# Kernel tuning notes

Measured on AMD Instinct MI355X. Metric: run time of the kernel, lower is better.

The kernel has to match this reference:

```python
import jax, jax.numpy as jnp
import numpy as np

N_NODES = 50000
IN_DIM = 256
LATENT = 128
HIDDEN = 2 * LATENT  # 256


def _xavier(key, fan_in, fan_out):
    # matches nn.init.xavier_uniform_ on a [out, in] weight; we store as [in, out]
    limit = float(np.sqrt(6.0 / (fan_in + fan_out)))
    return jax.random.uniform(key, (fan_in, fan_out), jnp.float32, -limit, limit)


def setup_inputs() -> dict:
    key = jax.random.key(0)
    ks = jax.random.split(key, 8)
    x = jax.random.normal(ks[0], (N_NODES, IN_DIM), jnp.float32)
    edge_index = jax.random.randint(ks[1], (2, 800000), 0, N_NODES, jnp.int64)
    W1 = _xavier(ks[2], IN_DIM, HIDDEN)
    b1 = jnp.zeros((HIDDEN,), jnp.float32)
    Wmu = _xavier(ks[3], HIDDEN, LATENT)
    bmu = jnp.zeros((LATENT,), jnp.float32)
    Wlv = _xavier(ks[4], HIDDEN, LATENT)
    blv = jnp.zeros((LATENT,), jnp.float32)
    return {"x": x, "edge_index": edge_index, "W1": W1, "b1": b1,
            "Wmu": Wmu, "bmu": bmu, "Wlv": Wlv, "blv": blv}


def _gcn_layer(x, W, b, src, dst):
    # PyG GCNConv: h = x @ W; add self loops; symmetric norm; scatter-add; + bias
    h = x @ W  # [N, out]
    ones = jnp.ones(src.shape[0], x.dtype)
    deg = jax.ops.segment_sum(ones, dst, num_segments=N_NODES) + 1.0  # +1 for self loop
    dinv = jax.lax.rsqrt(deg)  # deg >= 1 always
    norm = dinv[src] * dinv[dst]  # [E]
    agg = jax.ops.segment_sum(h[src] * norm[:, None], dst, num_segments=N_NODES)
    agg = agg + h * (dinv * dinv)[:, None]  # self-loop contribution, norm_ii = 1/deg_i
    return agg + b


def reference(x, edge_index, W1, b1, Wmu, bmu, Wlv, blv):
    src, dst = edge_index[0], edge_index[1]
    z = _gcn_layer(x, W1, b1, src, dst)
    z = jax.nn.relu(z)
    # dropout in eval mode == identity
    mu = _gcn_layer(z, Wmu, bmu, src, dst)
    logvar = _gcn_layer(z, Wlv, blv, src, dst)
    return (mu, logvar)
```

## Files before the change

### kernel.cpp

```cpp
#include <hip/hip_runtime.h>

#define N_NODES 50000
#define E_EDGES 800000
#define D 256
#define L 128
#define CAP 64

typedef __attribute__((ext_vector_type(8))) short bf16x8;
typedef __attribute__((ext_vector_type(4))) float f32x4;

__device__ __forceinline__ float bf2f(unsigned short u) {
    union { unsigned int i; float f; } v; v.i = ((unsigned int)u) << 16; return v.f;
}
__device__ __forceinline__ unsigned short f2bf(float f) {
    union { float f; unsigned int i; } v; v.f = f;
    unsigned int r = v.i + 0x7fffu + ((v.i >> 16) & 1u);
    return (unsigned short)(r >> 16);
}

__global__ __launch_bounds__(256) void zero_i(int* __restrict__ p, int n) {
    int i = blockIdx.x * 256 + threadIdx.x;
    if (i < n) p[i] = 0;
}

__global__ __launch_bounds__(256) void fill_fixed(const int* __restrict__ src,
                                                  const int* __restrict__ dst,
                                                  int* __restrict__ cursor,
                                                  int* __restrict__ bucket) {
    int e = blockIdx.x * 256 + threadIdx.x;
    if (e >= E_EDGES) return;
    int d = dst[e];
    int pos = atomicAdd(&cursor[d], 1);
    if (pos < CAP) bucket[d * CAP + pos] = src[e];
}

__global__ __launch_bounds__(256) void dinv_fin(const int* __restrict__ cursor,
                                                float* __restrict__ dinv) {
    int i = blockIdx.x * 256 + threadIdx.x;
    if (i < N_NODES) dinv[i] = rsqrtf((float)cursor[i] + 1.0f);
}

__global__ __launch_bounds__(256) void prep_w(
    const float* __restrict__ W1, const float* __restrict__ Wmu,
    const float* __restrict__ Wlv, const float* __restrict__ bmu,
    const float* __restrict__ blv,
    unsigned short* __restrict__ W1h, unsigned short* __restrict__ W1l,
    unsigned short* __restrict__ Wch, unsigned short* __restrict__ Wcl,
    float* __restrict__ bcat) {
    int b = blockIdx.x, t = threadIdx.x;
    if (b < 256) {
        int n = b, k = t;
        float w = W1[k * 256 + n];
        unsigned short h = f2bf(w);
        W1h[n * 256 + k] = h;
        W1l[n * 256 + k] = f2bf(w - bf2f(h));
    } else {
        int n = b - 256, k = t;
        float w = (n < 128) ? Wmu[k * 128 + n] : Wlv[k * 128 + (n - 128)];
        unsigned short h = f2bf(w);
        Wch[n * 256 + k] = h;
        Wcl[n * 256 + k] = f2bf(w - bf2f(h));
        if (b == 256) bcat[t] = (t < 128) ? bmu[t] : blv[t - 128];
    }
}

__global__ __launch_bounds__(256, 3) void gemm_mfma(
    const float* __restrict__ A,
    const unsigned short* __restrict__ Bth, const unsigned short* __restrict__ Btl,
    unsigned short* __restrict__ Hout,
    float* __restrict__ mu, float* __restrict__ lv,
    const float* __restrict__ bias, int M, int mode)
{
    __shared__ unsigned short Bsh[256 * 32];
    __shared__ unsigned short Bsl[256 * 32];
    const int t = threadIdx.x;
    const int lane = t & 63, wave = t >> 6;
    const int row0 = blockIdx.x * 64 + wave * 16;
    const int m_ = lane & 15, q = lane >> 4;
    int rA = row0 + m_; if (rA >= M) rA = M - 1;
    const float* Ap = A + (size_t)rA * 256;
    const int bn = t >> 2;
    const int bc = t & 3;

    f32x4 acc[16];
    const f32x4 zf = {0.f, 0.f, 0.f, 0.f};
#pragma unroll
    for (int nt = 0; nt < 16; ++nt) acc[nt] = zf;

    for (int ks = 0; ks < 8; ++ks) {
        const int k0 = ks * 32;
        bf16x8 gbh[4], gbl[4];
#pragma unroll
        for (int i = 0; i < 4; ++i) {
            int n = bn + i * 64;
            gbh[i] = *(const bf16x8*)(Bth + n * 256 + k0 + bc * 8);
            gbl[i] = *(const bf16x8*)(Btl + n * 256 + k0 + bc * 8);
        }
        float4 av0 = *(const float4*)(Ap + k0 + q * 8);
        float4 av1 = *(const float4*)(Ap + k0 + q * 8 + 4);
        __syncthreads();
#pragma unroll
        for (int i = 0; i < 4; ++i) {
            int n = bn + i * 64;
            int cc = (bc ^ ((n >> 1) & 3)) * 8;
            *(bf16x8*)&Bsh[n * 32 + cc] = gbh[i];
            *(bf16x8*)&Bsl[n * 32 + cc] = gbl[i];
        }
        float af[8] = {av0.x, av0.y, av0.z, av0.w, av1.x, av1.y, av1.z, av1.w};
        bf16x8 ah, al;
#pragma unroll
        for (int j = 0; j < 8; ++j) {
            unsigned short h = f2bf(af[j]);
            ah[j] = (short)h;
            al[j] = (short)f2bf(af[j] - bf2f(h));
        }
        __syncthreads();
#pragma unroll
        for (int nt = 0; nt < 16; ++nt) {
            int n = nt * 16 + m_;
            int cr = (q ^ ((n >> 1) & 3)) * 8;
            bf16x8 bh = *(const bf16x8*)&Bsh[n * 32 + cr];
            bf16x8 bl = *(const bf16x8*)&Bsl[n * 32 + cr];
            acc[nt] = __builtin_amdgcn_mfma_f32_16x16x32_bf16(ah, bh, acc[nt], 0, 0, 0);
            acc[nt] = __builtin_amdgcn_mfma_f32_16x16x32_bf16(ah, bl, acc[nt], 0, 0, 0);
            acc[nt] = __builtin_amdgcn_mfma_f32_16x16x32_bf16(al, bh, acc[nt], 0, 0, 0);
        }
    }
    int rbase = row0 + q * 4;
#pragma unroll
    for (int r = 0; r < 4; ++r) {
        int grow = rbase + r;
        if (grow >= M) continue;
#pragma unroll
        for (int nt = 0; nt < 16; ++nt) {
            int gcol = nt * 16 + m_;
            float v = acc[nt][r];
            if (mode == 0) {
                Hout[(size_t)grow * 256 + gcol] = f2bf(v);
            } else {
                v += bias[gcol];
                if (gcol < 128) mu[(size_t)grow * 128 + gcol] = v;
                else            lv[(size_t)grow * 128 + (gcol - 128)] = v;
            }
        }
    }
}

__global__ __launch_bounds__(256) void gather_pre(
    const unsigned short* __restrict__ Hs,
    const int* __restrict__ bucket, const int* __restrict__ cnt_,
    const float* __restrict__ dinv, const float* __restrict__ bias,
    unsigned short* __restrict__ OutZ, float* __restrict__ OutY, int mode)
{
    const int lane = threadIdx.x & 63;
    const int hl = lane & 31;
    const int bb = lane & 32;
    const int node = blockIdx.x * 8 + (threadIdx.x >> 5);
    const int col = hl * 8;
    int cnt = cnt_[node]; if (cnt > CAP) cnt = CAP;
    float dn = dinv[node];

    int   s0r = 0, s1r = 0;
    float w0r = 0.f, w1r = 0.f;
    if (hl < cnt)      { s0r = bucket[node * CAP + hl];      w0r = dinv[s0r] * dn; }
    if (hl + 32 < cnt) { s1r = bucket[node * CAP + 32 + hl]; w1r = dinv[s1r] * dn; }

    float sl = dn * dn;
    bf16x8 hv = *(const bf16x8*)(Hs + (size_t)node * D + col);
    float a[8];
#pragma unroll
    for (int p = 0; p < 8; ++p) a[p] = bf2f((unsigned short)hv[p]) * sl;

    const int cnt0 = cnt < 32 ? cnt : 32;
    int j = 0;
    for (; j + 3 < cnt0; j += 4) {
        int t0 = __shfl(s0r, bb + j,     64), t1 = __shfl(s0r, bb + j + 1, 64);
        int t2 = __shfl(s0r, bb + j + 2, 64), t3 = __shfl(s0r, bb + j + 3, 64);
        float w0 = __shfl(w0r, bb + j,     64), w1 = __shfl(w0r, bb + j + 1, 64);
        float w2 = __shfl(w0r, bb + j + 2, 64), w3 = __shfl(w0r, bb + j + 3, 64);
        bf16x8 u0 = *(const bf16x8*)(Hs + (size_t)t0 * D + col);
        bf16x8 u1 = *(const bf16x8*)(Hs + (size_t)t1 * D + col);
        bf16x8 u2 = *(const bf16x8*)(Hs + (size_t)t2 * D + col);
        bf16x8 u3 = *(const bf16x8*)(Hs + (size_t)t3 * D + col);
#pragma unroll
        for (int p = 0; p < 8; ++p) a[p] = fmaf(bf2f((unsigned short)u0[p]), w0, a[p]);
#pragma unroll
        for (int p = 0; p < 8; ++p) a[p] = fmaf(bf2f((unsigned short)u1[p]), w1, a[p]);
#pragma unroll
        for (int p = 0; p < 8; ++p) a[p] = fmaf(bf2f((unsigned short)u2[p]), w2, a[p]);
#pragma unroll
        for (int p = 0; p < 8; ++p) a[p] = fmaf(bf2f((unsigned short)u3[p]), w3, a[p]);
    }
    for (; j < cnt0; ++j) {
        int   t0 = __shfl(s0r, bb + j, 64);
        float w0 = __shfl(w0r, bb + j, 64);
        bf16x8 u0 = *(const bf16x8*)(Hs + (size_t)t0 * D + col);
#pragma unroll
        for (int p = 0; p < 8; ++p) a[p] = fmaf(bf2f((unsigned short)u0[p]), w0, a[p]);
    }
    if (cnt > 32) {
        for (int j2 = 0; j2 < cnt - 32; ++j2) {
            int   t0 = __shfl(s1r, bb + j2, 64);
            float w0 = __shfl(w1r, bb + j2, 64);
            bf16x8 u0 = *(const bf16x8*)(Hs + (size_t)t0 * D + col);
#pragma unroll
            for (int p = 0; p < 8; ++p) a[p] = fmaf(bf2f((unsigned short)u0[p]), w0, a[p]);
        }
    }

    if (mode == 0) {
        float4 b0 = *(const float4*)(bias + col);
        float4 b1 = *(const float4*)(bias + col + 4);
        float bf[8] = {b0.x, b0.y, b0.z, b0.w, b1.x, b1.y, b1.z, b1.w};
        bf16x8 o;
#pragma unroll
        for (int p = 0; p < 8; ++p) o[p] = (short)f2bf(fmaxf(a[p] + bf[p], 0.f));
        *(bf16x8*)(OutZ + (size_t)node * D + col) = o;
    } else {
        float4 o0, o1;
        o0.x = a[0]; o0.y = a[1]; o0.z = a[2]; o0.w = a[3];
        o1.x = a[4]; o1.y = a[5]; o1.z = a[6]; o1.w = a[7];
        float* Yp = OutY + (size_t)node * D + col;
        *(float4*)Yp = o0;
        *(float4*)(Yp + 4) = o1;
    }
}

extern "C" void kernel_launch(void* const* d_in, const int* in_sizes, int n_in,
                              void* d_out, int out_size, void* d_ws, size_t ws_size,
                              hipStream_t stream) {
    const float* x   = (const float*)d_in[0];
    const int*   ei  = (const int*)d_in[1];
    const float* W1  = (const float*)d_in[2];
    const float* b1  = (const float*)d_in[3];
    const float* Wmu = (const float*)d_in[4];
    const float* bmu = (const float*)d_in[5];
    const float* Wlv = (const float*)d_in[6];
    const float* blv = (const float*)d_in[7];
    const int* src = ei;
    const int* dst = ei + E_EDGES;

    const size_t NF = (size_t)N_NODES * D;
    unsigned short* Hb = (unsigned short*)d_ws;
    unsigned short* Z  = Hb + NF;
    float* Y = (float*)(Z + NF);
    unsigned short* W1h = (unsigned short*)(Y + NF);
    unsigned short* W1l = W1h + 65536;
    unsigned short* Wch = W1l + 65536;
    unsigned short* Wcl = Wch + 65536;
    float* bcat = (float*)(Wcl + 65536);
    float* dinv = bcat + 256;
    int* cursor = (int*)(dinv + N_NODES);
    int* bucket = cursor + N_NODES;
    float* mu = (float*)d_out;
    float* lv = mu + (size_t)N_NODES * L;

    zero_i<<<(N_NODES + 255) / 256, 256, 0, stream>>>(cursor, N_NODES);
    fill_fixed<<<(E_EDGES + 255) / 256, 256, 0, stream>>>(src, dst, cursor, bucket);
    dinv_fin<<<(N_NODES + 255) / 256, 256, 0, stream>>>(cursor, dinv);

    prep_w<<<512, 256, 0, stream>>>(W1, Wmu, Wlv, bmu, blv, W1h, W1l, Wch, Wcl, bcat);

    const int gemm_blocks = (N_NODES + 63) / 64;
    const int gat_blocks  = N_NODES / 8;
    gemm_mfma<<<gemm_blocks, 256, 0, stream>>>(x, W1h, W1l, Hb,
                                               nullptr, nullptr, nullptr, N_NODES, 0);
    gather_pre<<<gat_blocks, 256, 0, stream>>>(Hb, bucket, cursor, dinv, b1,
                                               Z, nullptr, 0);
    gather_pre<<<gat_blocks, 256, 0, stream>>>(Z, bucket, cursor, dinv, nullptr,
                                               nullptr, Y, 1);
    gemm_mfma<<<gemm_blocks, 256, 0, stream>>>(Y, Wch, Wcl, nullptr,
                                               mu, lv, bcat, N_NODES, 1);
}
```

Baseline: 345.3 us.

## Column-slice gather with packed fp16 edge weights in bucket entries

```diff
diff --git a/kernel.cpp b/kernel.cpp
--- a/kernel.cpp
+++ b/kernel.cpp
@@ -5,6 +5,7 @@
 #define D 256
 #define L 128
 #define CAP 64
+#define SCOL 32
 
 typedef __attribute__((ext_vector_type(8))) short bf16x8;
 typedef __attribute__((ext_vector_type(4))) float f32x4;
@@ -16,6 +17,17 @@
     union { float f; unsigned int i; } v; v.f = f;
     unsigned int r = v.i + 0x7fffu + ((v.i >> 16) & 1u);
     return (unsigned short)(r >> 16);
+}
+__device__ __forceinline__ unsigned short f2h(float f) {
+    union { float f; unsigned int i; } v; v.f = f;
+    unsigned int r = v.i - 0x38000000u;
+    r = r + 0xfffu + ((r >> 13) & 1u);
+    return (unsigned short)(r >> 13);
+}
+__device__ __forceinline__ float h2f(unsigned int u) {
+    union { unsigned int i; float f; } v;
+    v.i = ((u & 0x7fffu) << 13) + 0x38000000u;
+    return v.f;
 }
 
 __global__ __launch_bounds__(256) void zero_i(int* __restrict__ p, int n) {
@@ -38,6 +50,21 @@
                                                 float* __restrict__ dinv) {
     int i = blockIdx.x * 256 + threadIdx.x;
     if (i < N_NODES) dinv[i] = rsqrtf((float)cursor[i] + 1.0f);
+}
+
+__global__ __launch_bounds__(256) void pack_bucket(int* __restrict__ bucket,
+                                                   const int* __restrict__ cnt_,
+                                                   const float* __restrict__ dinv) {
+    int node = blockIdx.x * 4 + (threadIdx.x >> 6);
+    if (node >= N_NODES) return;
+    int lane = threadIdx.x & 63;
+    int cnt = cnt_[node]; if (cnt > CAP) cnt = CAP;
+    if (lane < cnt) {
+        int idx = node * CAP + lane;
+        int s = bucket[idx];
+        unsigned short wh = f2h(dinv[s] * dinv[node]);
+        bucket[idx] = (s & 0xffff) | ((int)wh << 16);
+    }
 }
 
 __global__ __launch_bounds__(256) void prep_w(
@@ -146,42 +173,41 @@
     }
 }
 
-__global__ __launch_bounds__(256) void gather_pre(
+__global__ __launch_bounds__(256) void gather_slice(
     const unsigned short* __restrict__ Hs,
-    const int* __restrict__ bucket, const int* __restrict__ cnt_,
+    const int* __restrict__ epk, const int* __restrict__ cnt_,
     const float* __restrict__ dinv, const float* __restrict__ bias,
     unsigned short* __restrict__ OutZ, float* __restrict__ OutY, int mode)
 {
-    const int lane = threadIdx.x & 63;
-    const int hl = lane & 31;
-    const int bb = lane & 32;
-    const int node = blockIdx.x * 8 + (threadIdx.x >> 5);
-    const int col = hl * 8;
+    const int s = blockIdx.x & 7;
+    const int g = blockIdx.x >> 3;
+    const int t = threadIdx.x;
+    const int node = g * 64 + ((t >> 6) << 4) + ((t & 63) >> 2);
+    if (node >= N_NODES) return;
+    const int r = t & 3;
+    const int col = s * SCOL + r * 8;
     int cnt = cnt_[node]; if (cnt > CAP) cnt = CAP;
-    float dn = dinv[node];
-
-    int   s0r = 0, s1r = 0;
-    float w0r = 0.f, w1r = 0.f;
-    if (hl < cnt)      { s0r = bucket[node * CAP + hl];      w0r = dinv[s0r] * dn; }
-    if (hl + 32 < cnt) { s1r = bucket[node * CAP + 32 + hl]; w1r = dinv[s1r] * dn; }
-
-    float sl = dn * dn;
-    bf16x8 hv = *(const bf16x8*)(Hs + (size_t)node * D + col);
+    const float dn = dinv[node];
+    const unsigned short* Hp = Hs + col;
+
     float a[8];
-#pragma unroll
-    for (int p = 0; p < 8; ++p) a[p] = bf2f((unsigned short)hv[p]) * sl;
-
-    const int cnt0 = cnt < 32 ? cnt : 32;
+    {
+        bf16x8 hv = *(const bf16x8*)(Hp + (size_t)node * D);
+        float sl = dn * dn;
+#pragma unroll
+        for (int p = 0; p < 8; ++p) a[p] = bf2f((unsigned short)hv[p]) * sl;
+    }
+
+    const int* ep = epk + node * CAP;
     int j = 0;
-    for (; j + 3 < cnt0; j += 4) {
-        int t0 = __shfl(s0r, bb + j,     64), t1 = __shfl(s0r, bb + j + 1, 64);
-        int t2 = __shfl(s0r, bb + j + 2, 64), t3 = __shfl(s0r, bb + j + 3, 64);
-        float w0 = __shfl(w0r, bb + j,     64), w1 = __shfl(w0r, bb + j + 1, 64);
-        float w2 = __shfl(w0r, bb + j + 2, 64), w3 = __shfl(w0r, bb + j + 3, 64);
-        bf16x8 u0 = *(const bf16x8*)(Hs + (size_t)t0 * D + col);
-        bf16x8 u1 = *(const bf16x8*)(Hs + (size_t)t1 * D + col);
-        bf16x8 u2 = *(const bf16x8*)(Hs + (size_t)t2 * D + col);
-        bf16x8 u3 = *(const bf16x8*)(Hs + (size_t)t3 * D + col);
+    for (; j + 3 < cnt; j += 4) {
+        int v0 = ep[j], v1 = ep[j + 1], v2 = ep[j + 2], v3 = ep[j + 3];
+        bf16x8 u0 = *(const bf16x8*)(Hp + (size_t)(v0 & 0xffff) * D);
+        bf16x8 u1 = *(const bf16x8*)(Hp + (size_t)(v1 & 0xffff) * D);
+        bf16x8 u2 = *(const bf16x8*)(Hp + (size_t)(v2 & 0xffff) * D);
+        bf16x8 u3 = *(const bf16x8*)(Hp + (size_t)(v3 & 0xffff) * D);
+        float w0 = h2f((unsigned int)v0 >> 16), w1 = h2f((unsigned int)v1 >> 16);
+        float w2 = h2f((unsigned int)v2 >> 16), w3 = h2f((unsigned int)v3 >> 16);
 #pragma unroll
         for (int p = 0; p < 8; ++p) a[p] = fmaf(bf2f((unsigned short)u0[p]), w0, a[p]);
 #pragma unroll
@@ -191,21 +217,12 @@
 #pragma unroll
         for (int p = 0; p < 8; ++p) a[p] = fmaf(bf2f((unsigned short)u3[p]), w3, a[p]);
     }
-    for (; j < cnt0; ++j) {
-        int   t0 = __shfl(s0r, bb + j, 64);
-        float w0 = __shfl(w0r, bb + j, 64);
-        bf16x8 u0 = *(const bf16x8*)(Hs + (size_t)t0 * D + col);
+    for (; j < cnt; ++j) {
+        int v0 = ep[j];
+        bf16x8 u0 = *(const bf16x8*)(Hp + (size_t)(v0 & 0xffff) * D);
+        float w0 = h2f((unsigned int)v0 >> 16);
 #pragma unroll
         for (int p = 0; p < 8; ++p) a[p] = fmaf(bf2f((unsigned short)u0[p]), w0, a[p]);
-    }
-    if (cnt > 32) {
-        for (int j2 = 0; j2 < cnt - 32; ++j2) {
-            int   t0 = __shfl(s1r, bb + j2, 64);
-            float w0 = __shfl(w1r, bb + j2, 64);
-            bf16x8 u0 = *(const bf16x8*)(Hs + (size_t)t0 * D + col);
-#pragma unroll
-            for (int p = 0; p < 8; ++p) a[p] = fmaf(bf2f((unsigned short)u0[p]), w0, a[p]);
-        }
     }
 
     if (mode == 0) {
@@ -258,17 +275,18 @@
     zero_i<<<(N_NODES + 255) / 256, 256, 0, stream>>>(cursor, N_NODES);
     fill_fixed<<<(E_EDGES + 255) / 256, 256, 0, stream>>>(src, dst, cursor, bucket);
     dinv_fin<<<(N_NODES + 255) / 256, 256, 0, stream>>>(cursor, dinv);
+    pack_bucket<<<(N_NODES + 3) / 4, 256, 0, stream>>>(bucket, cursor, dinv);
 
     prep_w<<<512, 256, 0, stream>>>(W1, Wmu, Wlv, bmu, blv, W1h, W1l, Wch, Wcl, bcat);
 
     const int gemm_blocks = (N_NODES + 63) / 64;
-    const int gat_blocks  = N_NODES / 8;
+    const int gat_blocks  = ((N_NODES + 63) / 64) * 8;
     gemm_mfma<<<gemm_blocks, 256, 0, stream>>>(x, W1h, W1l, Hb,
                                                nullptr, nullptr, nullptr, N_NODES, 0);
-    gather_pre<<<gat_blocks, 256, 0, stream>>>(Hb, bucket, cursor, dinv, b1,
-                                               Z, nullptr, 0);
-    gather_pre<<<gat_blocks, 256, 0, stream>>>(Z, bucket, cursor, dinv, nullptr,
-                                               nullptr, Y, 1);
+    gather_slice<<<gat_blocks, 256, 0, stream>>>(Hb, bucket, cursor, dinv, b1,
+                                                 Z, nullptr, 0);
+    gather_slice<<<gat_blocks, 256, 0, stream>>>(Z, bucket, cursor, dinv, nullptr,
+                                                 nullptr, Y, 1);
     gemm_mfma<<<gemm_blocks, 256, 0, stream>>>(Y, Wch, Wcl, nullptr,
                                                mu, lv, bcat, N_NODES, 1);
 }
```

Measured after the change: 434.1 us. +25.7%, slower.

## Reorder second layer to GEMM-then-aggregate with bf16 intermediate

Applied to the files above, without the earlier changes.

```diff
diff --git a/kernel.cpp b/kernel.cpp
--- a/kernel.cpp
+++ b/kernel.cpp
@@ -67,9 +67,7 @@
 __global__ __launch_bounds__(256, 3) void gemm_mfma(
     const float* __restrict__ A,
     const unsigned short* __restrict__ Bth, const unsigned short* __restrict__ Btl,
-    unsigned short* __restrict__ Hout,
-    float* __restrict__ mu, float* __restrict__ lv,
-    const float* __restrict__ bias, int M, int mode)
+    unsigned short* __restrict__ Hout, int M)
 {
     __shared__ unsigned short Bsh[256 * 32];
     __shared__ unsigned short Bsl[256 * 32];
@@ -134,14 +132,70 @@
 #pragma unroll
         for (int nt = 0; nt < 16; ++nt) {
             int gcol = nt * 16 + m_;
-            float v = acc[nt][r];
-            if (mode == 0) {
-                Hout[(size_t)grow * 256 + gcol] = f2bf(v);
-            } else {
-                v += bias[gcol];
-                if (gcol < 128) mu[(size_t)grow * 128 + gcol] = v;
-                else            lv[(size_t)grow * 128 + (gcol - 128)] = v;
-            }
+            Hout[(size_t)grow * 256 + gcol] = f2bf(acc[nt][r]);
+        }
+    }
+}
+
+__global__ __launch_bounds__(256, 3) void gemm_bf16(
+    const unsigned short* __restrict__ A,
+    const unsigned short* __restrict__ Bth, const unsigned short* __restrict__ Btl,
+    unsigned short* __restrict__ Tout, int M)
+{
+    __shared__ unsigned short Bsh[256 * 32];
+    __shared__ unsigned short Bsl[256 * 32];
+    const int t = threadIdx.x;
+    const int lane = t & 63, wave = t >> 6;
+    const int row0 = blockIdx.x * 64 + wave * 16;
+    const int m_ = lane & 15, q = lane >> 4;
+    int rA = row0 + m_; if (rA >= M) rA = M - 1;
+    const unsigned short* Ap = A + (size_t)rA * 256;
+    const int bn = t >> 2;
+    const int bc = t & 3;
+
+    f32x4 acc[16];
+    const f32x4 zf = {0.f, 0.f, 0.f, 0.f};
+#pragma unroll
+    for (int nt = 0; nt < 16; ++nt) acc[nt] = zf;
+
+    for (int ks = 0; ks < 8; ++ks) {
+        const int k0 = ks * 32;
+        bf16x8 gbh[4], gbl[4];
+#pragma unroll
+        for (int i = 0; i < 4; ++i) {
+            int n = bn + i * 64;
+            gbh[i] = *(const bf16x8*)(Bth + n * 256 + k0 + bc * 8);
+            gbl[i] = *(const bf16x8*)(Btl + n * 256 + k0 + bc * 8);
+        }
+        bf16x8 ah = *(const bf16x8*)(Ap + k0 + q * 8);
+        __syncthreads();
+#pragma unroll
+        for (int i = 0; i < 4; ++i) {
+            int n = bn + i * 64;
+            int cc = (bc ^ ((n >> 1) & 3)) * 8;
+            *(bf16x8*)&Bsh[n * 32 + cc] = gbh[i];
+            *(bf16x8*)&Bsl[n * 32 + cc] = gbl[i];
+        }
+        __syncthreads();
+#pragma unroll
+        for (int nt = 0; nt < 16; ++nt) {
+            int n = nt * 16 + m_;
+            int cr = (q ^ ((n >> 1) & 3)) * 8;
+            bf16x8 bh = *(const bf16x8*)&Bsh[n * 32 + cr];
+            bf16x8 bl = *(const bf16x8*)&Bsl[n * 32 + cr];
+            acc[nt] = __builtin_amdgcn_mfma_f32_16x16x32_bf16(ah, bh, acc[nt], 0, 0, 0);
+            acc[nt] = __builtin_amdgcn_mfma_f32_16x16x32_bf16(ah, bl, acc[nt], 0, 0, 0);
+        }
+    }
+    int rbase = row0 + q * 4;
+#pragma unroll
+    for (int r = 0; r < 4; ++r) {
+        int grow = rbase + r;
+        if (grow >= M) continue;
+#pragma unroll
+        for (int nt = 0; nt < 16; ++nt) {
+            int gcol = nt * 16 + m_;
+            Tout[(size_t)grow * 256 + gcol] = f2bf(acc[nt][r]);
         }
     }
 }
@@ -150,7 +204,8 @@
     const unsigned short* __restrict__ Hs,
     const int* __restrict__ bucket, const int* __restrict__ cnt_,
     const float* __restrict__ dinv, const float* __restrict__ bias,
-    unsigned short* __restrict__ OutZ, float* __restrict__ OutY, int mode)
+    unsigned short* __restrict__ OutZ,
+    float* __restrict__ mu, float* __restrict__ lv, int mode)
 {
     const int lane = threadIdx.x & 63;
     const int hl = lane & 31;
@@ -208,21 +263,24 @@
         }
     }
 
+    float4 b0 = *(const float4*)(bias + col);
+    float4 b1 = *(const float4*)(bias + col + 4);
+    float bf[8] = {b0.x, b0.y, b0.z, b0.w, b1.x, b1.y, b1.z, b1.w};
     if (mode == 0) {
-        float4 b0 = *(const float4*)(bias + col);
-        float4 b1 = *(const float4*)(bias + col + 4);
-        float bf[8] = {b0.x, b0.y, b0.z, b0.w, b1.x, b1.y, b1.z, b1.w};
         bf16x8 o;
 #pragma unroll
         for (int p = 0; p < 8; ++p) o[p] = (short)f2bf(fmaxf(a[p] + bf[p], 0.f));
         *(bf16x8*)(OutZ + (size_t)node * D + col) = o;
     } else {
         float4 o0, o1;
-        o0.x = a[0]; o0.y = a[1]; o0.z = a[2]; o0.w = a[3];
-        o1.x = a[4]; o1.y = a[5]; o1.z = a[6]; o1.w = a[7];
-        float* Yp = OutY + (size_t)node * D + col;
-        *(float4*)Yp = o0;
-        *(float4*)(Yp + 4) = o1;
+        o0.x = a[0] + bf[0]; o0.y = a[1] + bf[1];
+        o0.z = a[2] + bf[2]; o0.w = a[3] + bf[3];
+        o1.x = a[4] + bf[4]; o1.y = a[5] + bf[5];
+        o1.z = a[6] + bf[6]; o1.w = a[7] + bf[7];
+        float* Op = (col < 128) ? (mu + (size_t)node * L + col)
+                                : (lv + (size_t)node * L + (col - 128));
+        *(float4*)Op = o0;
+        *(float4*)(Op + 4) = o1;
     }
 }
 
@@ -243,8 +301,8 @@
     const size_t NF = (size_t)N_NODES * D;
     unsigned short* Hb = (unsigned short*)d_ws;
     unsigned short* Z  = Hb + NF;
-    float* Y = (float*)(Z + NF);
-    unsigned short* W1h = (unsigned short*)(Y + NF);
+    unsigned short* T  = Z + NF;
+    unsigned short* W1h = T + NF;
     unsigned short* W1l = W1h + 65536;
     unsigned short* Wch = W1l + 65536;
     unsigned short* Wcl = Wch + 65536;
@@ -263,12 +321,10 @@
 
     const int gemm_blocks = (N_NODES + 63) / 64;
     const int gat_blocks  = N_NODES / 8;
-    gemm_mfma<<<gemm_blocks, 256, 0, stream>>>(x, W1h, W1l, Hb,
-                                               nullptr, nullptr, nullptr, N_NODES, 0);
+    gemm_mfma<<<gemm_blocks, 256, 0, stream>>>(x, W1h, W1l, Hb, N_NODES);
     gather_pre<<<gat_blocks, 256, 0, stream>>>(Hb, bucket, cursor, dinv, b1,
-                                               Z, nullptr, 0);
-    gather_pre<<<gat_blocks, 256, 0, stream>>>(Z, bucket, cursor, dinv, nullptr,
-                                               nullptr, Y, 1);
-    gemm_mfma<<<gemm_blocks, 256, 0, stream>>>(Y, Wch, Wcl, nullptr,
-                                               mu, lv, bcat, N_NODES, 1);
-}
+                                               Z, nullptr, nullptr, 0);
+    gemm_bf16<<<gemm_blocks, 256, 0, stream>>>(Z, Wch, Wcl, T, N_NODES);
+    gather_pre<<<gat_blocks, 256, 0, stream>>>(T, bucket, cursor, dinv, bcat,
+                                               nullptr, mu, lv, 1);
+}
```

New measurement: 336.2 us. -2.6%, faster.
